# Kernel tuning notes

Hardware: AMD Instinct MI355X
Metric: run time of the kernel (lower is better)

The kernel has to match this reference:

```python
import jax, jax.numpy as jnp
import numpy as np
jax.config.update("jax_enable_x64", True)

IN_FEATURES = 4096
OUT_FEATURES = 4096
BATCH, SEQ = 4, 2048


def _gen_weight(seed, out_features, in_features):
    # Stand-in for the Rust FastGMemContext PRNG fill: deterministic fp64
    # weight regenerated from the 64-bit seed on every call (never stored).
    k = jax.random.key(seed)
    return jax.random.normal(k, (out_features, in_features), dtype=jnp.float64)


def setup_inputs() -> dict:
    key = jax.random.key(0)
    kx, _ = jax.random.split(key)
    x = jax.random.normal(kx, (BATCH, SEQ, IN_FEATURES), dtype=jnp.float32)
    bias = jnp.zeros((OUT_FEATURES,), dtype=jnp.float32)
    return {"x": x, "bias": bias, "seed": 42}


def reference(x, bias, seed):
    out_features = bias.shape[0]
    in_features = x.shape[-1]
    w = _gen_weight(seed, out_features, in_features)  # [out, in] fp64
    # fp64 matmul, downcast to input dtype, then add bias (as in GMemLinear)
    out = jnp.matmul(x.astype(jnp.float64), w.T).astype(x.dtype)
    return out + bias
```

## Files before the change

### kernel.cpp

```cpp
#include <hip/hip_runtime.h>
#include <hip/hip_bf16.h>
#include <cstdint>
#include <math.h>


typedef __bf16  bf16x8 __attribute__((ext_vector_type(8)));
typedef float   f32x4  __attribute__((ext_vector_type(4)));
typedef unsigned short u16x8 __attribute__((ext_vector_type(8)));

__device__ __forceinline__ unsigned short f2bf_rne(float f) {
  uint32_t x = __float_as_uint(f);
  uint32_t r = (x + 0x7FFFu + ((x >> 16) & 1u)) >> 16;
  return (unsigned short)r;
}

__device__ __forceinline__ void threefry2x32(uint32_t k0, uint32_t k1,
                                             uint32_t x0, uint32_t x1,
                                             uint32_t& o0, uint32_t& o1) {
  uint32_t ks0 = k0, ks1 = k1, ks2 = k0 ^ k1 ^ 0x1BD11BDAu;
  uint32_t ks[3] = {ks0, ks1, ks2};
  x0 += ks0; x1 += ks1;
  const uint32_t rot0[4] = {13u, 15u, 26u, 6u};
  const uint32_t rot1[4] = {17u, 29u, 16u, 24u};
#pragma unroll
  for (int i = 0; i < 5; ++i) {
    const uint32_t* r = (i & 1) ? rot1 : rot0;
#pragma unroll
    for (int j = 0; j < 4; ++j) {
      x0 += x1;
      x1 = (x1 << r[j]) | (x1 >> (32u - r[j]));
      x1 ^= x0;
    }
    x0 += ks[(i + 1) % 3];
    x1 += ks[(i + 2) % 3] + (uint32_t)(i + 1);
  }
  o0 = x0; o1 = x1;
}

__device__ __forceinline__ double erfinv_mixed(double u) {
  double au = fabs(u);
  double t  = (1.0 - au) * (1.0 + au);
  float  wf = -logf((float)t);
  if (wf < 15.5f) {
    float w, p;
    if (wf < 5.0f) {
      w = wf - 2.5f;
      p = 2.81022636e-08f;
      p = 3.43273939e-07f + p * w;
      p = -3.5233877e-06f + p * w;
      p = -4.39150654e-06f + p * w;
      p = 0.00021858087f + p * w;
      p = -0.00125372503f + p * w;
      p = -0.00417768164f + p * w;
      p = 0.246640727f + p * w;
      p = 1.50140941f + p * w;
    } else {
      w = sqrtf(wf) - 3.0f;
      p = -0.000200214257f;
      p = 0.000100950558f + p * w;
      p = 0.00134934322f + p * w;
      p = -0.00367342844f + p * w;
      p = 0.00573950773f + p * w;
      p = -0.0076224613f + p * w;
      p = 0.00943887047f + p * w;
      p = 1.00167406f + p * w;
      p = 2.83297682f + p * w;
    }
    return (double)(p * (float)u);
  } else {
    double L = -log(1.0 - au);
    double r = sqrt(L);
    r = sqrt(L - log(r) - 0.5723649429247001);
    r = sqrt(L - log(r) - 0.5723649429247001);
    return (u < 0.0) ? -r : r;
  }
}

__global__ void gen_and_cast(const float* __restrict__ X,
                             unsigned short* __restrict__ Y,
                             unsigned short* __restrict__ W,
                             const int* __restrict__ seedp,
                             int nx, int nw) {
  const int tid = (int)threadIdx.x;
  if (blockIdx.x < 2048) {
    const int n8 = nx >> 3;
    const int stride = 2048 * 256;
    for (int q = (int)(blockIdx.x * 256 + tid); q < n8; q += stride) {
      const float4* p = (const float4*)(X + ((size_t)q << 3));
      float4 a = p[0], b = p[1];
      u16x8 o;
      o[0] = f2bf_rne(a.x); o[1] = f2bf_rne(a.y);
      o[2] = f2bf_rne(a.z); o[3] = f2bf_rne(a.w);
      o[4] = f2bf_rne(b.x); o[5] = f2bf_rne(b.y);
      o[6] = f2bf_rne(b.z); o[7] = f2bf_rne(b.w);
      *(u16x8*)(Y + ((size_t)q << 3)) = o;
    }
  } else {
    const uint32_t k1 = (uint32_t)seedp[0];
    const uint32_t k0 = 0u;
    const double DLO = -0x1.fffffffffffffp-1;
    const int nq = nw >> 2;
    const int stride = 6144 * 256;
    for (int q = (int)((blockIdx.x - 2048) * 256 + tid); q < nq; q += stride) {
      ushort4 outv;
      unsigned short tmp[4];
#pragma unroll
      for (int j = 0; j < 4; ++j) {
        uint32_t e = ((uint32_t)q << 2) + (uint32_t)j;
        uint32_t o0, o1;
        threefry2x32(k0, k1, 0u, e, o0, o1);
        uint64_t bits = ((uint64_t)o0 << 32) | (uint64_t)o1;
        uint64_t fb = (bits >> 12) | 0x3FF0000000000000ull;
        union { uint64_t u; double d; } cv; cv.u = fb;
        double f = cv.d - 1.0;
        double u = f * 2.0 + DLO;
        u = fmax(u, DLO);
        double x = erfinv_mixed(u);
        float wv = (float)(1.4142135623730951 * x);
        tmp[j] = f2bf_rne(wv);
      }
      outv.x = tmp[0]; outv.y = tmp[1]; outv.z = tmp[2]; outv.w = tmp[3];
      *(ushort4*)(W + ((size_t)q << 2)) = outv;
    }
  }
}


__device__ __forceinline__ void gload_lds16(const void* g, void* l) {
  __builtin_amdgcn_global_load_lds(
      (const __attribute__((address_space(1))) unsigned int*)g,
      (__attribute__((address_space(3))) unsigned int*)l, 16, 0, 0);
}

__device__ __forceinline__ uint32_t lds_u32(void* p) {
  return (uint32_t)(uintptr_t)(__attribute__((address_space(3))) char*)p;
}

template <int OFF>
__device__ __forceinline__ bf16x8 dsr16(uint32_t a) {
  bf16x8 r;
  asm volatile("ds_read_b128 %0, %1 offset:%2" : "=v"(r) : "v"(a), "i"(OFF));
  return r;
}

__global__ __launch_bounds__(512, 2) void gemm256(
    const unsigned short* __restrict__ A,
    const unsigned short* __restrict__ B,
    const float* __restrict__ bias,
    float* __restrict__ C,
    int M, int N, int K) {
  __shared__ __align__(1024) char lds[131072];

  const int nwg = (int)gridDim.x;
  int wg = (int)blockIdx.x;
  wg = (wg & 7) * (nwg >> 3) + (wg >> 3);
  const int ntn = N >> 8;
  const int tm = wg / ntn, tn = wg - tm * ntn;

  const int tid = (int)threadIdx.x;
  const int w = tid >> 6, l = tid & 63;
  const int wr = w >> 2, wc = w & 3;
  const int l15 = l & 15;

  int laneRd = (l15 << 6) | ((l >> 4) << 4);
  laneRd ^= ((l15 >> 1) & 3) << 4;
  const int stRow = l >> 2;
  const int stCol = (((l & 3) ^ ((l >> 3) & 3)) << 4);

  const char* Ag = (const char*)A;
  const char* Bg = (const char*)B;
  const long rowA0 = (long)tm * 256;
  const long rowB0 = (long)tn * 256;
  const long Kb = (long)K;

  const uint32_t lds0  = lds_u32(&lds[0]);
  const uint32_t aBase = lds0 + (uint32_t)(wr * 8192 + laneRd);
  const uint32_t bBase = lds0 + 16384u + (uint32_t)(wc * 4096 + laneRd);

#define STAGE_A(kt_, cs_)                                                     \
  _Pragma("unroll")                                                           \
  for (int i_ = 0; i_ < 2; ++i_) {                                            \
    const int u_ = w * 2 + i_;                                                \
    gload_lds16(Ag + 2 * ((rowA0 + u_ * 16 + stRow) * Kb + (long)(kt_) * 32) + stCol, \
                &lds[(cs_) * 32768 + u_ * 1024]);                             \
  }
#define STAGE_B(kt_, cs_)                                                     \
  _Pragma("unroll")                                                           \
  for (int i_ = 0; i_ < 2; ++i_) {                                            \
    const int u_ = w * 2 + i_;                                                \
    gload_lds16(Bg + 2 * ((rowB0 + u_ * 16 + stRow) * Kb + (long)(kt_) * 32) + stCol, \
                &lds[(cs_) * 32768 + 16384 + u_ * 1024]);                     \
  }

#define MFMA16(base_)                                                         \
  _Pragma("unroll")                                                           \
  for (int mi = 0; mi < 4; ++mi)                                              \
    _Pragma("unroll")                                                         \
    for (int ni = 0; ni < 4; ++ni)                                            \
      acc[(base_) + mi][ni] = __builtin_amdgcn_mfma_f32_16x16x32_bf16(        \
          aq[mi], bq[ni], acc[(base_) + mi][ni], 0, 0, 0);

#define TILE_BODY(c_, kt_, vm_, st_)                                          \
  {                                                                           \
    const uint32_t aB = aBase + (c_) * 32768u;                                \
    const uint32_t bB = bBase + (c_) * 32768u;                                \
    bf16x8 aq[4], bq[4];                                                      \
    bq[0] = dsr16<0>(bB);    bq[1] = dsr16<1024>(bB);                         \
    bq[2] = dsr16<2048>(bB); bq[3] = dsr16<3072>(bB);                         \
    aq[0] = dsr16<0>(aB);    aq[1] = dsr16<1024>(aB);                         \
    aq[2] = dsr16<2048>(aB); aq[3] = dsr16<3072>(aB);                         \
    if (st_) { STAGE_A((kt_) + 3, ((c_) + 3) & 3) }                           \
    __builtin_amdgcn_s_barrier();                                             \
    asm volatile("s_waitcnt lgkmcnt(0)" ::: "memory");                        \
    __builtin_amdgcn_sched_barrier(0);                                        \
    __builtin_amdgcn_s_setprio(1);                                            \
    MFMA16(0)                                                                 \
    __builtin_amdgcn_s_setprio(0);                                            \
    aq[0] = dsr16<4096>(aB); aq[1] = dsr16<5120>(aB);                         \
    aq[2] = dsr16<6144>(aB); aq[3] = dsr16<7168>(aB);                         \
    if (st_) { STAGE_B((kt_) + 3, ((c_) + 3) & 3) }                           \
    asm volatile("s_waitcnt lgkmcnt(0)" ::: "memory");                        \
    __builtin_amdgcn_sched_barrier(0);                                        \
    __builtin_amdgcn_s_setprio(1);                                            \
    MFMA16(4)                                                                 \
    __builtin_amdgcn_s_setprio(0);                                            \
    asm volatile("s_waitcnt vmcnt(" #vm_ ")" ::: "memory");                   \
    __builtin_amdgcn_sched_barrier(0);                                        \
    __builtin_amdgcn_s_barrier();                                             \
  }

  f32x4 acc[8][4];
#pragma unroll
  for (int i = 0; i < 8; ++i)
#pragma unroll
    for (int j = 0; j < 4; ++j) acc[i][j] = (f32x4){0.f, 0.f, 0.f, 0.f};

  const int NTt = K >> 5;

  STAGE_A(0, 0) STAGE_B(0, 0)
  STAGE_A(1, 1) STAGE_B(1, 1)
  STAGE_A(2, 2) STAGE_B(2, 2)
  asm volatile("s_waitcnt vmcnt(8)" ::: "memory");
  __builtin_amdgcn_sched_barrier(0);
  __builtin_amdgcn_s_barrier();

  int kt = 0;
  for (; kt + 7 < NTt; kt += 4) {
    TILE_BODY(0, kt,     8, 1)
    TILE_BODY(1, kt + 1, 8, 1)
    TILE_BODY(2, kt + 2, 8, 1)
    TILE_BODY(3, kt + 3, 8, 1)
  }
  TILE_BODY(0, kt,     8, 1)
  TILE_BODY(1, kt + 1, 4, 0)
  TILE_BODY(2, kt + 2, 0, 0)
  TILE_BODY(3, kt + 3, 0, 0)

#pragma unroll
  for (int ni = 0; ni < 4; ++ni) {
    const int col = tn * 256 + wc * 64 + ni * 16 + l15;
    const float bv = bias[col];
#pragma unroll
    for (int mi = 0; mi < 8; ++mi) {
      const int r0 = tm * 256 + wr * 128 + mi * 16 + ((l >> 4) << 2);
      f32x4 v = acc[mi][ni];
#pragma unroll
      for (int j = 0; j < 4; ++j)
        C[(size_t)(r0 + j) * N + col] = v[j] + bv;
    }
  }
#undef STAGE_A
#undef STAGE_B
#undef MFMA16
#undef TILE_BODY
}

extern "C" void kernel_launch(void* const* d_in, const int* in_sizes, int n_in,
                              void* d_out, int out_size, void* d_ws, size_t ws_size,
                              hipStream_t stream) {
  const float* x    = (const float*)d_in[0];
  const float* bias = (const float*)d_in[1];
  const int*   seed = (const int*)d_in[2];
  float* out = (float*)d_out;

  const int K = 4096;
  const int N = in_sizes[1];
  const int M = in_sizes[0] / K;

  unsigned short* W  = (unsigned short*)d_ws;
  unsigned short* Xb = W + (size_t)N * K;

  gen_and_cast<<<8192, 256, 0, stream>>>(x, Xb, W, seed, M * K, N * K);

  dim3 grid((M / 256) * (N / 256));
  gemm256<<<grid, 512, 0, stream>>>((const unsigned short*)Xb,
                                    (const unsigned short*)W,
                                    bias, out, M, N, K);
}
```

Before: 314.9 us.

## Compute weight normals in fp32, interleave cast/gen blocks, prefetch all A fragments

The weight generator now derives the uniform and erfinv in fp32 with fast log intrinsics instead of fp64 arithmetic, removing costly double-precision math on the RNG path. Cast and generation blocks are interleaved by block index so both kinds of work are spread across the GPU. In the GEMM tile body, all eight A fragments are loaded up front, the first barrier is dropped, and a partial lgkmcnt wait lets the first MFMA group start while later loads are still in flight. The fp32 path may change some generated weights slightly near the tails, and removing the barrier could race with the stage writes into the LDS buffer.

```diff
diff --git a/kernel.cpp b/kernel.cpp
--- a/kernel.cpp
+++ b/kernel.cpp
@@ -37,10 +37,16 @@
   o0 = x0; o1 = x1;
 }
 
-__device__ __forceinline__ double erfinv_mixed(double u) {
-  double au = fabs(u);
-  double t  = (1.0 - au) * (1.0 + au);
-  float  wf = -logf((float)t);
+__device__ __forceinline__ float normal_from_bits(uint64_t m52) {
+  float f = (float)m52 * 0x1p-52f;
+  float u = 2.0f * f - 1.0f;
+  uint64_t dmin_i = (m52 >= (1ull << 51)) ? ((1ull << 52) - m52) : m52;
+  float dminf = fmaxf((float)dmin_i, 0.25f);
+  float oma = dminf * 0x1p-51f;
+  float opa = 2.0f - oma;
+  float t = oma * opa;
+  float wf = -__logf(t);
+  float x;
   if (wf < 15.5f) {
     float w, p;
     if (wf < 5.0f) {
@@ -66,14 +72,15 @@
       p = 1.00167406f + p * w;
       p = 2.83297682f + p * w;
     }
-    return (double)(p * (float)u);
+    x = p * u;
   } else {
-    double L = -log(1.0 - au);
-    double r = sqrt(L);
-    r = sqrt(L - log(r) - 0.5723649429247001);
-    r = sqrt(L - log(r) - 0.5723649429247001);
-    return (u < 0.0) ? -r : r;
-  }
+    float L = wf + __logf(opa);
+    float r = sqrtf(L);
+    r = sqrtf(L - __logf(r) - 0.57236494f);
+    r = sqrtf(L - __logf(r) - 0.57236494f);
+    x = (u < 0.0f) ? -r : r;
+  }
+  return 1.41421356f * x;
 }
 
 __global__ void gen_and_cast(const float* __restrict__ X,
@@ -82,10 +89,11 @@
                              const int* __restrict__ seedp,
                              int nx, int nw) {
   const int tid = (int)threadIdx.x;
-  if (blockIdx.x < 2048) {
+  const int bid = (int)blockIdx.x;
+  if ((bid & 3) == 0) {
     const int n8 = nx >> 3;
     const int stride = 2048 * 256;
-    for (int q = (int)(blockIdx.x * 256 + tid); q < n8; q += stride) {
+    for (int q = (int)((bid >> 2) * 256 + tid); q < n8; q += stride) {
       const float4* p = (const float4*)(X + ((size_t)q << 3));
       float4 a = p[0], b = p[1];
       u16x8 o;
@@ -98,10 +106,10 @@
   } else {
     const uint32_t k1 = (uint32_t)seedp[0];
     const uint32_t k0 = 0u;
-    const double DLO = -0x1.fffffffffffffp-1;
     const int nq = nw >> 2;
+    const int gidx = bid - (bid >> 2) - 1;
     const int stride = 6144 * 256;
-    for (int q = (int)((blockIdx.x - 2048) * 256 + tid); q < nq; q += stride) {
+    for (int q = gidx * 256 + tid; q < nq; q += stride) {
       ushort4 outv;
       unsigned short tmp[4];
 #pragma unroll
@@ -110,14 +118,7 @@
         uint32_t o0, o1;
         threefry2x32(k0, k1, 0u, e, o0, o1);
         uint64_t bits = ((uint64_t)o0 << 32) | (uint64_t)o1;
-        uint64_t fb = (bits >> 12) | 0x3FF0000000000000ull;
-        union { uint64_t u; double d; } cv; cv.u = fb;
-        double f = cv.d - 1.0;
-        double u = f * 2.0 + DLO;
-        u = fmax(u, DLO);
-        double x = erfinv_mixed(u);
-        float wv = (float)(1.4142135623730951 * x);
-        tmp[j] = f2bf_rne(wv);
+        tmp[j] = f2bf_rne(normal_from_bits(bits >> 12));
       }
       outv.x = tmp[0]; outv.y = tmp[1]; outv.z = tmp[2]; outv.w = tmp[3];
       *(ushort4*)(W + ((size_t)q << 2)) = outv;
@@ -198,26 +199,25 @@
     _Pragma("unroll")                                                         \
     for (int ni = 0; ni < 4; ++ni)                                            \
       acc[(base_) + mi][ni] = __builtin_amdgcn_mfma_f32_16x16x32_bf16(        \
-          aq[mi], bq[ni], acc[(base_) + mi][ni], 0, 0, 0);
+          aq[(base_) + mi], bq[ni], acc[(base_) + mi][ni], 0, 0, 0);
 
 #define TILE_BODY(c_, kt_, vm_, st_)                                          \
   {                                                                           \
     const uint32_t aB = aBase + (c_) * 32768u;                                \
     const uint32_t bB = bBase + (c_) * 32768u;                                \
-    bf16x8 aq[4], bq[4];                                                      \
+    bf16x8 aq[8], bq[4];                                                      \
     bq[0] = dsr16<0>(bB);    bq[1] = dsr16<1024>(bB);                         \
     bq[2] = dsr16<2048>(bB); bq[3] = dsr16<3072>(bB);                         \
     aq[0] = dsr16<0>(aB);    aq[1] = dsr16<1024>(aB);                         \
     aq[2] = dsr16<2048>(aB); aq[3] = dsr16<3072>(aB);                         \
+    aq[4] = dsr16<4096>(aB); aq[5] = dsr16<5120>(aB);                         \
+    aq[6] = dsr16<6144>(aB); aq[7] = dsr16<7168>(aB);                         \
     if (st_) { STAGE_A((kt_) + 3, ((c_) + 3) & 3) }                           \
-    __builtin_amdgcn_s_barrier();                                             \
-    asm volatile("s_waitcnt lgkmcnt(0)" ::: "memory");                        \
+    asm volatile("s_waitcnt lgkmcnt(4)" ::: "memory");                        \
     __builtin_amdgcn_sched_barrier(0);                                        \
     __builtin_amdgcn_s_setprio(1);                                            \
     MFMA16(0)                                                                 \
     __builtin_amdgcn_s_setprio(0);                                            \
-    aq[0] = dsr16<4096>(aB); aq[1] = dsr16<5120>(aB);                         \
-    aq[2] = dsr16<6144>(aB); aq[3] = dsr16<7168>(aB);                         \
     if (st_) { STAGE_B((kt_) + 3, ((c_) + 3) & 3) }                           \
     asm volatile("s_waitcnt lgkmcnt(0)" ::: "memory");                        \
     __builtin_amdgcn_sched_barrier(0);                                        \
```

Result: no change. 318.7 us (+1.2%).
